# Optimization experiments

Measured on AMD Instinct MI355X. Metric: run time of the kernel, lower is better.

The kernel has to match this reference:

```python
import jax, jax.numpy as jnp
import numpy as np

D_MODEL = 1024
N_HEADS = 16
D_HEAD = D_MODEL // N_HEADS
HIDDEN = 4096
B, T = 2, 2048
EPS = 1e-5


def setup_inputs() -> dict:
    key = jax.random.key(0)
    ks = jax.random.split(key, 16)
    s = 0.02
    return {
        "x": jax.random.normal(ks[0], (B, T, D_MODEL), dtype=jnp.float32),
        # LayerNorm 1
        "gamma1": jnp.ones((D_MODEL,), jnp.float32),
        "beta1": jnp.zeros((D_MODEL,), jnp.float32),
        # attention projections, stored (in, out) so y = x @ W + b
        "Wq": jax.random.normal(ks[1], (D_MODEL, D_MODEL), jnp.float32) * s,
        "bq": jnp.zeros((D_MODEL,), jnp.float32),
        "Wk": jax.random.normal(ks[2], (D_MODEL, D_MODEL), jnp.float32) * s,
        "bk": jnp.zeros((D_MODEL,), jnp.float32),
        "Wv": jax.random.normal(ks[3], (D_MODEL, D_MODEL), jnp.float32) * s,
        "bv": jnp.zeros((D_MODEL,), jnp.float32),
        "Wo": jax.random.normal(ks[4], (D_MODEL, D_MODEL), jnp.float32) * s,
        "bo": jnp.zeros((D_MODEL,), jnp.float32),
        # LayerNorm 2
        "gamma2": jnp.ones((D_MODEL,), jnp.float32),
        "beta2": jnp.zeros((D_MODEL,), jnp.float32),
        # MLP
        "W1": jax.random.normal(ks[5], (D_MODEL, HIDDEN), jnp.float32) * s,
        "b1": jnp.zeros((HIDDEN,), jnp.float32),
        "W2": jax.random.normal(ks[6], (HIDDEN, D_MODEL), jnp.float32) * s,
        "b2": jnp.zeros((D_MODEL,), jnp.float32),
    }


def _layernorm(x, gamma, beta):
    mean = jnp.mean(x, axis=-1, keepdims=True)
    var = jnp.mean(jnp.square(x - mean), axis=-1, keepdims=True)  # unbiased=False
    return gamma * (x - mean) * jax.lax.rsqrt(var + EPS) + beta


def _attention(x, Wq, bq, Wk, bk, Wv, bv, Wo, bo):
    b, t, _ = x.shape
    q = (x @ Wq + bq).reshape(b, t, N_HEADS, D_HEAD)
    k = (x @ Wk + bk).reshape(b, t, N_HEADS, D_HEAD)
    v = (x @ Wv + bv).reshape(b, t, N_HEADS, D_HEAD)
    scores = jnp.einsum("bqhd,bkhd->bhqk", q, k) / np.sqrt(D_HEAD).astype(np.float32)
    causal = jnp.tril(jnp.ones((t, t), dtype=bool))  # keep j <= i
    scores = jnp.where(causal, scores, -jnp.inf)
    attn = jax.nn.softmax(scores, axis=-1)
    out = jnp.einsum("bhqk,bkhd->bqhd", attn, v).reshape(b, t, D_MODEL)
    return out @ Wo + bo


def reference(x, gamma1, beta1, Wq, bq, Wk, bk, Wv, bv, Wo, bo,
              gamma2, beta2, W1, b1, W2, b2):
    # x = x + Attn(LN1(x))
    x = x + _attention(_layernorm(x, gamma1, beta1), Wq, bq, Wk, bk, Wv, bv, Wo, bo)
    # x = x + MLP(LN2(x)); torch F.gelu default = exact erf gelu
    h = _layernorm(x, gamma2, beta2)
    h = jax.nn.gelu(h @ W1 + b1, approximate=False) @ W2 + b2
    return x + h
```

## Files before the change

kernel.cpp:

```cpp
#include <hip/hip_runtime.h>
#include <stdint.h>

typedef unsigned short u16;
typedef short bf16x8 __attribute__((ext_vector_type(8)));
typedef float f32x4 __attribute__((ext_vector_type(4)));
typedef float f32x16 __attribute__((ext_vector_type(16)));

#define MB (1024L*1024L)

__device__ inline u16 f2bf(float f) {
  union { float f; unsigned u; } v; v.f = f;
  unsigned r = (v.u + 0x7FFFu + ((v.u >> 16) & 1u)) >> 16;
  return (u16)r;
}

__device__ inline float bf2f(u16 u) {
  union { unsigned u; float f; } v; v.u = ((unsigned)u) << 16; return v.f;
}

__device__ inline unsigned cvtpk(float lo, float hi) {
  unsigned r;
  asm("v_cvt_pk_bf16_f32 %0, %1, %2" : "=v"(r) : "v"(lo), "v"(hi));
  return r;
}

#define GLOAD16(gptr, lptr) \
  __builtin_amdgcn_global_load_lds((__attribute__((address_space(1))) void*)(gptr), \
                                   (__attribute__((address_space(3))) void*)(lptr), 16, 0, 0)

__global__ __launch_bounds__(256) void twconv(const float* __restrict__ W,
                                              u16* __restrict__ WT, int K, int N) {
  __shared__ float tile[32][33];
  const int nbn = N >> 5;
  const int bk = blockIdx.x / nbn;
  const int bn = blockIdx.x % nbn;
  const int tid = threadIdx.x;
  const int r = tid >> 3;
  const int c4 = (tid & 7) << 2;
  const float4 v = *(const float4*)(W + (size_t)(bk * 32 + r) * N + bn * 32 + c4);
  tile[r][c4 + 0] = v.x; tile[r][c4 + 1] = v.y;
  tile[r][c4 + 2] = v.z; tile[r][c4 + 3] = v.w;
  __syncthreads();
  ushort4 o;
  o.x = f2bf(tile[c4 + 0][r]); o.y = f2bf(tile[c4 + 1][r]);
  o.z = f2bf(tile[c4 + 2][r]); o.w = f2bf(tile[c4 + 3][r]);
  *(ushort4*)(WT + (size_t)(bn * 32 + r) * K + bk * 32 + c4) = o;
}

__global__ __launch_bounds__(256) void concat3(const float* __restrict__ a,
                                               const float* __restrict__ b,
                                               const float* __restrict__ c,
                                               float* __restrict__ out, int n) {
  int i = blockIdx.x * 256 + threadIdx.x;
  if (i < n) { out[i] = a[i]; out[n + i] = b[i]; out[2 * n + i] = c[i]; }
}

__global__ __launch_bounds__(256) void ln_kernel(const float* __restrict__ x,
                                                 const float* __restrict__ gamma,
                                                 const float* __restrict__ beta,
                                                 u16* __restrict__ out) {
  const int row = blockIdx.x;
  const int tid = threadIdx.x;
  const float4 v = *(const float4*)(x + (size_t)row * 1024 + tid * 4);
  float s = v.x + v.y + v.z + v.w;
  float s2 = v.x * v.x + v.y * v.y + v.z * v.z + v.w * v.w;
#pragma unroll
  for (int m = 1; m < 64; m <<= 1) {
    s += __shfl_xor(s, m, 64);
    s2 += __shfl_xor(s2, m, 64);
  }
  __shared__ float red[8];
  const int w = tid >> 6;
  if ((tid & 63) == 0) { red[w] = s; red[4 + w] = s2; }
  __syncthreads();
  s = red[0] + red[1] + red[2] + red[3];
  s2 = red[4] + red[5] + red[6] + red[7];
  const float mean = s * (1.0f / 1024.0f);
  const float var = s2 * (1.0f / 1024.0f) - mean * mean;
  const float rstd = rsqrtf(var + 1e-5f);
  const float4 g = *(const float4*)(gamma + tid * 4);
  const float4 b = *(const float4*)(beta + tid * 4);
  ushort4 o;
  o.x = f2bf(g.x * (v.x - mean) * rstd + b.x);
  o.y = f2bf(g.y * (v.y - mean) * rstd + b.y);
  o.z = f2bf(g.z * (v.z - mean) * rstd + b.z);
  o.w = f2bf(g.w * (v.w - mean) * rstd + b.w);
  *(ushort4*)(out + (size_t)row * 1024 + tid * 4) = o;
}

template <int EPI, int BN>
__global__ __launch_bounds__(256, (BN == 64) ? 3 : 2)
void gemm_bt(const u16* __restrict__ A, const u16* __restrict__ BT,
             const float* __restrict__ bias, const float* __restrict__ res,
             void* __restrict__ outp, int M, int N, int K) {
  constexpr int MF = (BN == 128) ? 4 : 2;
  constexpr int ACH = 4;
  constexpr int BCH = BN / 32;
  constexpr int LOADS = ACH + BCH;
  __shared__ __align__(16) u16 As[2][128 * 64];
  __shared__ __align__(16) u16 Bs[2][BN * 64];
  const int nBN = N / BN;
  const int hw = blockIdx.x;
  const int xcd = hw & 7;
  const int rr = hw >> 3;
  const int bm = xcd * 4 + rr / nBN;
  const int bn = rr % nBN;
  const int tid = threadIdx.x;
  const int lane = tid & 63;
  const int wid = tid >> 6;
  const int wm = (BN == 128) ? (wid >> 1) : wid;
  const int wn = (BN == 128) ? (wid & 1) : 0;
  const int e4 = lane >> 4;

  int abase[MF], ax[MF];
#pragma unroll
  for (int m = 0; m < MF; ++m) {
    int rowa = wm * (MF * 16) + m * 16 + (lane & 15);
    abase[m] = rowa * 64; ax[m] = rowa & 7;
  }
  int bbase[4], bx[4];
#pragma unroll
  for (int n = 0; n < 4; ++n) {
    int rowb = wn * 64 + n * 16 + (lane & 15);
    bbase[n] = rowb * 64; bx[n] = rowb & 7;
  }

  size_t ga[ACH]; int loa[ACH];
#pragma unroll
  for (int c = 0; c < ACH; ++c) {
    int idx = tid + (c << 8);
    int row = idx >> 3;
    int ch = (idx & 7) ^ (row & 7);
    ga[c] = (size_t)(bm * 128 + row) * K + (ch << 3);
    loa[c] = idx << 4;
  }
  size_t gb[BCH]; int lob[BCH];
#pragma unroll
  for (int c = 0; c < BCH; ++c) {
    int idx = tid + (c << 8);
    int row = idx >> 3;
    int ch = (idx & 7) ^ (row & 7);
    gb[c] = (size_t)(bn * BN + row) * K + (ch << 3);
    lob[c] = idx << 4;
  }

#define STAGE_G(t, bb) do { \
  _Pragma("unroll") for (int c = 0; c < ACH; ++c) \
    GLOAD16(A + ga[c] + (size_t)(t) * 64, (char*)As[bb] + loa[c]); \
  _Pragma("unroll") for (int c = 0; c < BCH; ++c) \
    GLOAD16(BT + gb[c] + (size_t)(t) * 64, (char*)Bs[bb] + lob[c]); \
} while (0)

  f32x4 acc[MF][4] = {};
  const int nt = K >> 6;

  STAGE_G(0, 0);
  STAGE_G(1, 1);

  for (int t = 0; t < nt; ++t) {
    if (t + 1 < nt) {
      asm volatile("s_waitcnt vmcnt(%0)" :: "i"(LOADS) : "memory");
    } else {
      asm volatile("s_waitcnt vmcnt(0)" ::: "memory");
    }
    __builtin_amdgcn_s_barrier();
    const u16* Ap = As[t & 1];
    const u16* Bp = Bs[t & 1];
    bf16x8 af[2][MF], bfr[2][4];
#pragma unroll
    for (int kk = 0; kk < 2; ++kk) {
#pragma unroll
      for (int m = 0; m < MF; ++m)
        af[kk][m] = *(const bf16x8*)(Ap + abase[m] + (((((kk << 2) | e4)) ^ ax[m]) << 3));
#pragma unroll
      for (int n = 0; n < 4; ++n)
        bfr[kk][n] = *(const bf16x8*)(Bp + bbase[n] + (((((kk << 2) | e4)) ^ bx[n]) << 3));
    }
    asm volatile("s_waitcnt lgkmcnt(0)" ::: "memory");
    __builtin_amdgcn_s_barrier();
    if (t + 2 < nt) STAGE_G(t + 2, t & 1);
    __builtin_amdgcn_s_setprio(1);
#pragma unroll
    for (int kk = 0; kk < 2; ++kk)
#pragma unroll
      for (int m = 0; m < MF; ++m)
#pragma unroll
        for (int n = 0; n < 4; ++n)
          acc[m][n] = __builtin_amdgcn_mfma_f32_16x16x32_bf16(af[kk][m], bfr[kk][n], acc[m][n], 0, 0, 0);
    __builtin_amdgcn_s_setprio(0);
  }
#undef STAGE_G

  const int rbase = bm * 128 + wm * (MF * 16);
  const int cbase = bn * BN + wn * 64;
#pragma unroll
  for (int m = 0; m < MF; ++m) {
#pragma unroll
    for (int n = 0; n < 4; ++n) {
      const int col = cbase + n * 16 + (lane & 15);
      const int row0 = rbase + m * 16 + ((lane >> 4) << 2);
      const float bv = bias[col];
#pragma unroll
      for (int r = 0; r < 4; ++r) {
        const int row = row0 + r;
        float v = acc[m][n][r] + bv;
        if (EPI == 1) {
          ((float*)outp)[(size_t)row * N + col] = v + res[(size_t)row * N + col];
        } else if (EPI == 2) {
          float tt = v * (1.0f + 0.044715f * v * v);
          float sg = 1.0f / (1.0f + __expf(-1.5957691216057308f * tt));
          ((u16*)outp)[(size_t)row * N + col] = f2bf(v * sg);
        } else {
          ((u16*)outp)[(size_t)row * N + col] = f2bf(v);
        }
      }
    }
  }
}

__global__ __launch_bounds__(256, 3) void attn_kernel(const u16* __restrict__ QKV,
                                                      u16* __restrict__ O) {
  __shared__ __align__(16) u16 KV[4][4096];
  const int T = 2048, LD = 3072;
  const int hw = blockIdx.x;
  const int xcd = hw & 7;
  const int rr = hw >> 3;
  const int bh = xcd + 8 * (rr >> 4);
  const int p = rr & 15;
  const int b = bh >> 4, hd = bh & 15;
  const int tid = threadIdx.x;
  const int lane = tid & 63;
  const int w = tid >> 6;
  const int h = lane >> 5;
  const int cA = p, cB = 31 - p;
  const int myc = (w < 2) ? cA : cB;
  const int qwb = myc * 64 + (w & 1) * 32;
  const int qg = qwb + (lane & 31);
  const int myNt = myc + 1;
  const int nt = cB + 1;

  const u16* Qb = QKV + (size_t)b * T * LD + hd * 64;
  const u16* Kb = Qb + 1024;
  const u16* Vb = Qb + 2048;

  const float QSC = 0.18033688011112042f;
  bf16x8 qf[4];
#pragma unroll
  for (int s = 0; s < 4; ++s) {
    bf16x8 raw = *(const bf16x8*)(Qb + (size_t)qg * LD + s * 16 + h * 8);
    union { unsigned wd[4]; bf16x8 v; } u;
#pragma unroll
    for (int e = 0; e < 4; ++e)
      u.wd[e] = cvtpk(bf2f((u16)raw[2 * e]) * QSC, bf2f((u16)raw[2 * e + 1]) * QSC);
    qf[s] = u.v;
  }

  f32x16 oacc[2] = {};
  float m = -INFINITY, l = 0.0f;

  int krow[2], kgc[2], vrow[2], vcol[2];
#pragma unroll
  for (int c2 = 0; c2 < 2; ++c2) {
    int idx = tid + (c2 << 8);
    krow[c2] = idx >> 3;
    kgc[c2] = ((idx & 7) ^ (krow[c2] & 7)) << 3;
    vrow[c2] = idx >> 3;
    vcol[c2] = idx & 7;
  }

#pragma unroll
  for (int c2 = 0; c2 < 2; ++c2) {
    GLOAD16(Kb + (size_t)krow[c2] * LD + kgc[c2], (char*)KV[0] + (tid + (c2 << 8)) * 16);
    bf16x8 vv0 = *(const bf16x8*)(Vb + (size_t)vrow[c2] * LD + vcol[c2] * 8);
#pragma unroll
    for (int e = 0; e < 8; ++e) {
      int d = vcol[c2] * 8 + e;
      KV[2][(d << 6) | (vrow[c2] & 7) | ((((vrow[c2] >> 3) ^ e ^ vcol[c2]) & 7) << 3)] = (u16)vv0[e];
    }
  }
  __syncthreads();

  int cur = 0;
  for (int j = 0; j < nt; ++j) {
    const bool pre = (j + 1 < nt);
    bf16x8 vv[2];
    if (pre) {
#pragma unroll
      for (int c2 = 0; c2 < 2; ++c2) {
        GLOAD16(Kb + (size_t)((j + 1) * 64 + krow[c2]) * LD + kgc[c2],
                (char*)KV[cur ^ 1] + (tid + (c2 << 8)) * 16);
        vv[c2] = *(const bf16x8*)(Vb + (size_t)((j + 1) * 64 + vrow[c2]) * LD + vcol[c2] * 8);
      }
    }

    if (j < myNt) {
      f32x16 sacc[2] = {};
      const u16* Kp = KV[cur];
#pragma unroll
      for (int t = 0; t < 2; ++t) {
#pragma unroll
        for (int s = 0; s < 4; ++s) {
          int row = t * 32 + (lane & 31);
          bf16x8 kf = *(const bf16x8*)(Kp + (row << 6) + ((((2 * s + h) ^ (row & 7)) & 7) << 3));
          sacc[t] = __builtin_amdgcn_mfma_f32_32x32x16_bf16(kf, qf[s], sacc[t], 0, 0, 0);
        }
      }

      if (j == myc) {
#pragma unroll
        for (int t = 0; t < 2; ++t)
#pragma unroll
          for (int r = 0; r < 16; ++r) {
            int key = (j << 6) + 32 * t + (r & 3) + 8 * (r >> 2) + 4 * h;
            if (key > qg) sacc[t][r] = -INFINITY;
          }
      }

      float pmax = -INFINITY;
#pragma unroll
      for (int t = 0; t < 2; ++t)
#pragma unroll
        for (int r = 0; r < 16; ++r) pmax = fmaxf(pmax, sacc[t][r]);
      pmax = fmaxf(pmax, __shfl_xor(pmax, 32, 64));

      if (!__all(pmax - m <= 2.8853900817779268f)) {
        float mn = fmaxf(m, pmax);
        float alpha = exp2f(m - mn);
        m = mn;
        l *= alpha;
#pragma unroll
        for (int d2 = 0; d2 < 2; ++d2)
#pragma unroll
          for (int r = 0; r < 16; ++r) oacc[d2][r] *= alpha;
      }

      float lsum = 0.0f;
#pragma unroll
      for (int t = 0; t < 2; ++t)
#pragma unroll
        for (int r = 0; r < 16; ++r) {
          float pe = exp2f(sacc[t][r] - m);
          sacc[t][r] = pe;
          lsum += pe;
        }
      lsum += __shfl_xor(lsum, 32, 64);
      l += lsum;

      union PF { unsigned wd[4]; bf16x8 v; } pf[4];
#pragma unroll
      for (int t = 0; t < 2; ++t) {
#pragma unroll
        for (int kb = 0; kb < 2; ++kb) {
          int base = 8 * kb;
          unsigned A0 = cvtpk(sacc[t][base + 0], sacc[t][base + 1]);
          unsigned A2 = cvtpk(sacc[t][base + 2], sacc[t][base + 3]);
          unsigned A4 = cvtpk(sacc[t][base + 4], sacc[t][base + 5]);
          unsigned A6 = cvtpk(sacc[t][base + 6], sacc[t][base + 7]);
          unsigned S0 = (unsigned)__shfl_xor((int)(h ? A0 : A4), 32, 64);
          unsigned S2 = (unsigned)__shfl_xor((int)(h ? A2 : A6), 32, 64);
          PF& u = pf[2 * t + kb];
          u.wd[0] = h ? S0 : A0;
          u.wd[1] = h ? S2 : A2;
          u.wd[2] = h ? A4 : S0;
          u.wd[3] = h ? A6 : S2;
        }
      }

      const u16* Vp = KV[2 + cur];
#pragma unroll
      for (int d2 = 0; d2 < 2; ++d2) {
        int d = d2 * 32 + (lane & 31);
#pragma unroll
        for (int ks = 0; ks < 4; ++ks) {
          bf16x8 vf = *(const bf16x8*)(Vp + (d << 6) + ((((2 * ks + h) ^ (d & 7) ^ ((d >> 3) & 7)) & 7) << 3));
          oacc[d2] = __builtin_amdgcn_mfma_f32_32x32x16_bf16(vf, pf[ks].v, oacc[d2], 0, 0, 0);
        }
      }
    }

    if (pre) {
#pragma unroll
      for (int c2 = 0; c2 < 2; ++c2)
#pragma unroll
        for (int e = 0; e < 8; ++e) {
          int d = vcol[c2] * 8 + e;
          KV[2 + (cur ^ 1)][(d << 6) | (vrow[c2] & 7) | ((((vrow[c2] >> 3) ^ e ^ vcol[c2]) & 7) << 3)] = (u16)vv[c2][e];
        }
    }
    __syncthreads();
    cur ^= 1;
  }

  const float rinv = 1.0f / l;
  u16* Ob = (u16*)KV;
  const int qloc = w * 32 + (lane & 31);
#pragma unroll
  for (int d2 = 0; d2 < 2; ++d2)
#pragma unroll
    for (int r = 0; r < 16; ++r) {
      int d = d2 * 32 + (r & 3) + 8 * (r >> 2) + 4 * h;
      Ob[(qloc << 6) | (d ^ ((qloc & 7) << 3))] = f2bf(oacc[d2][r] * rinv);
    }
  __syncthreads();
#pragma unroll
  for (int it = 0; it < 4; ++it) {
    int r = (tid >> 3) + it * 32;
    int c = tid & 7;
    bf16x8 val = *(const bf16x8*)(Ob + (r << 6) + (((c ^ (r & 7)) & 7) << 3));
    int qg2 = (r < 64) ? (cA * 64 + r) : (cB * 64 + (r - 64));
    *(bf16x8*)(O + (size_t)(b * T + qg2) * 1024 + hd * 64 + c * 8) = val;
  }
}

extern "C" void kernel_launch(void* const* d_in, const int* in_sizes, int n_in,
                              void* d_out, int out_size, void* d_ws, size_t ws_size,
                              hipStream_t stream) {
  const float* x      = (const float*)d_in[0];
  const float* gamma1 = (const float*)d_in[1];
  const float* beta1  = (const float*)d_in[2];
  const float* Wq     = (const float*)d_in[3];
  const float* bq     = (const float*)d_in[4];
  const float* Wk     = (const float*)d_in[5];
  const float* bk     = (const float*)d_in[6];
  const float* Wv     = (const float*)d_in[7];
  const float* bv     = (const float*)d_in[8];
  const float* Wo     = (const float*)d_in[9];
  const float* bo     = (const float*)d_in[10];
  const float* gamma2 = (const float*)d_in[11];
  const float* beta2  = (const float*)d_in[12];
  const float* W1     = (const float*)d_in[13];
  const float* b1     = (const float*)d_in[14];
  const float* W2     = (const float*)d_in[15];
  const float* b2     = (const float*)d_in[16];

  char* ws = (char*)d_ws;
  u16* WqkvT = (u16*)(ws + 0 * MB);
  u16* WoT   = (u16*)(ws + 6 * MB);
  u16* W1T   = (u16*)(ws + 8 * MB);
  u16* W2T   = (u16*)(ws + 16 * MB);
  u16* qkv   = (u16*)(ws + 24 * MB);
  u16* hb    = (u16*)(ws + 24 * MB);
  u16* xn    = (u16*)(ws + 56 * MB);
  float* bqkv = (float*)d_out;
  float* x1 = (float*)d_out;

  const int M = 4096;

  twconv<<<dim3(1024), dim3(256), 0, stream>>>(Wq, WqkvT, 1024, 1024);
  twconv<<<dim3(1024), dim3(256), 0, stream>>>(Wk, WqkvT + 1024 * 1024, 1024, 1024);
  twconv<<<dim3(1024), dim3(256), 0, stream>>>(Wv, WqkvT + 2048 * 1024, 1024, 1024);
  twconv<<<dim3(1024), dim3(256), 0, stream>>>(Wo, WoT, 1024, 1024);
  twconv<<<dim3(4096), dim3(256), 0, stream>>>(W1, W1T, 1024, 4096);
  twconv<<<dim3(4096), dim3(256), 0, stream>>>(W2, W2T, 4096, 1024);
  concat3<<<dim3(4), dim3(256), 0, stream>>>(bq, bk, bv, bqkv, 1024);

  ln_kernel<<<dim3(M), dim3(256), 0, stream>>>(x, gamma1, beta1, xn);

  gemm_bt<0, 128><<<dim3(768), dim3(256), 0, stream>>>(xn, WqkvT, bqkv, nullptr, qkv, M, 3072, 1024);

  attn_kernel<<<dim3(512), dim3(256), 0, stream>>>(qkv, xn);

  gemm_bt<1, 64><<<dim3(512), dim3(256), 0, stream>>>(xn, WoT, bo, x, x1, M, 1024, 1024);

  ln_kernel<<<dim3(M), dim3(256), 0, stream>>>(x1, gamma2, beta2, xn);

  gemm_bt<2, 128><<<dim3(1024), dim3(256), 0, stream>>>(xn, W1T, b1, nullptr, hb, M, 4096, 1024);
  gemm_bt<1, 64><<<dim3(512), dim3(256), 0, stream>>>(hb, W2T, b2, x1, d_out, M, 1024, 4096);
}
```

Baseline: 254.3 us.

## Enlarge attention tiles to 128 queries/keys with 512-thread blocks

Restructures the causal flash-attention kernel so each block has 8 waves covering two 128-row query chunks, and processes 128-key K/V tiles per iteration instead of 64. The V transpose swizzle is widened to 16 groups for the new row stride, and the block-to-head mapping is changed so each XCD handles 4 heads. s_setprio is raised around the MFMA sections. The aim is more K/V reuse per shared-memory load and fewer barriers. The cost is a grid of only 256 blocks, which may leave CUs underused, plus more LDS and registers per block.

Result: no change. 252.3 us (-0.8%).

```diff
diff --git a/kernel.cpp b/kernel.cpp
--- a/kernel.cpp
+++ b/kernel.cpp
@@ -218,24 +218,24 @@
   }
 }
 
-__global__ __launch_bounds__(256, 3) void attn_kernel(const u16* __restrict__ QKV,
+__global__ __launch_bounds__(512, 2) void attn_kernel(const u16* __restrict__ QKV,
                                                       u16* __restrict__ O) {
-  __shared__ __align__(16) u16 KV[4][4096];
+  __shared__ __align__(16) u16 Ks[2][8192];
+  __shared__ __align__(16) u16 Vt[2][8192];
   const int T = 2048, LD = 3072;
-  const int hw = blockIdx.x;
-  const int xcd = hw & 7;
-  const int rr = hw >> 3;
-  const int bh = xcd + 8 * (rr >> 4);
-  const int p = rr & 15;
+  const int blk = blockIdx.x;
+  const int xcd = blk & 7;
+  const int idx = blk >> 3;
+  const int bh = xcd * 4 + (idx & 3);
+  const int p = idx >> 2;
   const int b = bh >> 4, hd = bh & 15;
   const int tid = threadIdx.x;
   const int lane = tid & 63;
   const int w = tid >> 6;
   const int h = lane >> 5;
-  const int cA = p, cB = 31 - p;
-  const int myc = (w < 2) ? cA : cB;
-  const int qwb = myc * 64 + (w & 1) * 32;
-  const int qg = qwb + (lane & 31);
+  const int cA = p, cB = 15 - p;
+  const int myc = (w < 4) ? cA : cB;
+  const int qg = myc * 128 + (w & 3) * 32 + (lane & 31);
   const int myNt = myc + 1;
   const int nt = cB + 1;
 
@@ -261,22 +261,25 @@
   int krow[2], kgc[2], vrow[2], vcol[2];
 #pragma unroll
   for (int c2 = 0; c2 < 2; ++c2) {
-    int idx = tid + (c2 << 8);
-    krow[c2] = idx >> 3;
-    kgc[c2] = ((idx & 7) ^ (krow[c2] & 7)) << 3;
-    vrow[c2] = idx >> 3;
-    vcol[c2] = idx & 7;
-  }
+    int i2 = tid + (c2 << 9);
+    krow[c2] = i2 >> 3;
+    kgc[c2] = ((i2 & 7) ^ (krow[c2] & 7)) << 3;
+    vrow[c2] = i2 >> 3;
+    vcol[c2] = i2 & 7;
+  }
+
+#define VWRITE(bb, c2, vvreg) do { \
+  _Pragma("unroll") for (int e = 0; e < 8; ++e) { \
+    int d = vcol[c2] * 8 + e; \
+    Vt[bb][(d << 7) | (vrow[c2] & 7) | ((((vrow[c2] >> 3) ^ (d & 15)) & 15) << 3)] = (u16)(vvreg)[e]; \
+  } \
+} while (0)
 
 #pragma unroll
   for (int c2 = 0; c2 < 2; ++c2) {
-    GLOAD16(Kb + (size_t)krow[c2] * LD + kgc[c2], (char*)KV[0] + (tid + (c2 << 8)) * 16);
+    GLOAD16(Kb + (size_t)krow[c2] * LD + kgc[c2], (char*)Ks[0] + (tid + (c2 << 9)) * 16);
     bf16x8 vv0 = *(const bf16x8*)(Vb + (size_t)vrow[c2] * LD + vcol[c2] * 8);
-#pragma unroll
-    for (int e = 0; e < 8; ++e) {
-      int d = vcol[c2] * 8 + e;
-      KV[2][(d << 6) | (vrow[c2] & 7) | ((((vrow[c2] >> 3) ^ e ^ vcol[c2]) & 7) << 3)] = (u16)vv0[e];
-    }
+    VWRITE(0, c2, vv0);
   }
   __syncthreads();
 
@@ -287,17 +290,18 @@
     if (pre) {
 #pragma unroll
       for (int c2 = 0; c2 < 2; ++c2) {
-        GLOAD16(Kb + (size_t)((j + 1) * 64 + krow[c2]) * LD + kgc[c2],
-                (char*)KV[cur ^ 1] + (tid + (c2 << 8)) * 16);
-        vv[c2] = *(const bf16x8*)(Vb + (size_t)((j + 1) * 64 + vrow[c2]) * LD + vcol[c2] * 8);
+        GLOAD16(Kb + (size_t)((j + 1) * 128 + krow[c2]) * LD + kgc[c2],
+                (char*)Ks[cur ^ 1] + (tid + (c2 << 9)) * 16);
+        vv[c2] = *(const bf16x8*)(Vb + (size_t)((j + 1) * 128 + vrow[c2]) * LD + vcol[c2] * 8);
       }
     }
 
     if (j < myNt) {
-      f32x16 sacc[2] = {};
-      const u16* Kp = KV[cur];
-#pragma unroll
-      for (int t = 0; t < 2; ++t) {
+      f32x16 sacc[4] = {};
+      const u16* Kp = Ks[cur];
+      __builtin_amdgcn_s_setprio(1);
+#pragma unroll
+      for (int t = 0; t < 4; ++t) {
 #pragma unroll
         for (int s = 0; s < 4; ++s) {
           int row = t * 32 + (lane & 31);
@@ -305,20 +309,21 @@
           sacc[t] = __builtin_amdgcn_mfma_f32_32x32x16_bf16(kf, qf[s], sacc[t], 0, 0, 0);
         }
       }
+      __builtin_amdgcn_s_setprio(0);
 
       if (j == myc) {
 #pragma unroll
-        for (int t = 0; t < 2; ++t)
+        for (int t = 0; t < 4; ++t)
 #pragma unroll
           for (int r = 0; r < 16; ++r) {
-            int key = (j << 6) + 32 * t + (r & 3) + 8 * (r >> 2) + 4 * h;
+            int key = (j << 7) + 32 * t + (r & 3) + 8 * (r >> 2) + 4 * h;
             if (key > qg) sacc[t][r] = -INFINITY;
           }
       }
 
       float pmax = -INFINITY;
 #pragma unroll
-      for (int t = 0; t < 2; ++t)
+      for (int t = 0; t < 4; ++t)
 #pragma unroll
         for (int r = 0; r < 16; ++r) pmax = fmaxf(pmax, sacc[t][r]);
       pmax = fmaxf(pmax, __shfl_xor(pmax, 32, 64));
@@ -336,7 +341,7 @@
 
       float lsum = 0.0f;
 #pragma unroll
-      for (int t = 0; t < 2; ++t)
+      for (int t = 0; t < 4; ++t)
 #pragma unroll
         for (int r = 0; r < 16; ++r) {
           float pe = exp2f(sacc[t][r] - m);
@@ -346,9 +351,9 @@
       lsum += __shfl_xor(lsum, 32, 64);
       l += lsum;
 
-      union PF { unsigned wd[4]; bf16x8 v; } pf[4];
-#pragma unroll
-      for (int t = 0; t < 2; ++t) {
+      union PF { unsigned wd[4]; bf16x8 v; } pf[8];
+#pragma unroll
+      for (int t = 0; t < 4; ++t) {
 #pragma unroll
         for (int kb = 0; kb < 2; ++kb) {
           int base = 8 * kb;
@@ -366,33 +371,31 @@
         }
       }
 
-      const u16* Vp = KV[2 + cur];
+      const u16* Vp = Vt[cur];
+      __builtin_amdgcn_s_setprio(1);
 #pragma unroll
       for (int d2 = 0; d2 < 2; ++d2) {
         int d = d2 * 32 + (lane & 31);
 #pragma unroll
-        for (int ks = 0; ks < 4; ++ks) {
-          bf16x8 vf = *(const bf16x8*)(Vp + (d << 6) + ((((2 * ks + h) ^ (d & 7) ^ ((d >> 3) & 7)) & 7) << 3));
+        for (int ks = 0; ks < 8; ++ks) {
+          bf16x8 vf = *(const bf16x8*)(Vp + (d << 7) + ((((2 * ks + h) ^ (d & 15)) & 15) << 3));
           oacc[d2] = __builtin_amdgcn_mfma_f32_32x32x16_bf16(vf, pf[ks].v, oacc[d2], 0, 0, 0);
         }
       }
+      __builtin_amdgcn_s_setprio(0);
     }
 
     if (pre) {
 #pragma unroll
-      for (int c2 = 0; c2 < 2; ++c2)
-#pragma unroll
-        for (int e = 0; e < 8; ++e) {
-          int d = vcol[c2] * 8 + e;
-          KV[2 + (cur ^ 1)][(d << 6) | (vrow[c2] & 7) | ((((vrow[c2] >> 3) ^ e ^ vcol[c2]) & 7) << 3)] = (u16)vv[c2][e];
-        }
+      for (int c2 = 0; c2 < 2; ++c2) VWRITE(cur ^ 1, c2, vv[c2]);
     }
     __syncthreads();
     cur ^= 1;
   }
+#undef VWRITE
 
   const float rinv = 1.0f / l;
-  u16* Ob = (u16*)KV;
+  u16* Ob = (u16*)Ks;
   const int qloc = w * 32 + (lane & 31);
 #pragma unroll
   for (int d2 = 0; d2 < 2; ++d2)
@@ -404,10 +407,10 @@
   __syncthreads();
 #pragma unroll
   for (int it = 0; it < 4; ++it) {
-    int r = (tid >> 3) + it * 32;
+    int r = (tid >> 3) + it * 64;
     int c = tid & 7;
     bf16x8 val = *(const bf16x8*)(Ob + (r << 6) + (((c ^ (r & 7)) & 7) << 3));
-    int qg2 = (r < 64) ? (cA * 64 + r) : (cB * 64 + (r - 64));
+    int qg2 = (r < 128) ? (cA * 128 + r) : (cB * 128 + (r - 128));
     *(bf16x8*)(O + (size_t)(b * T + qg2) * 1024 + hd * 64 + c * 8) = val;
   }
 }
@@ -458,7 +461,7 @@
 
   gemm_bt<0, 128><<<dim3(768), dim3(256), 0, stream>>>(xn, WqkvT, bqkv, nullptr, qkv, M, 3072, 1024);
 
-  attn_kernel<<<dim3(512), dim3(256), 0, stream>>>(qkv, xn);
+  attn_kernel<<<dim3(256), dim3(512), 0, stream>>>(qkv, xn);
 
   gemm_bt<1, 64><<<dim3(512), dim3(256), 0, stream>>>(xn, WoT, bo, x, x1, M, 1024, 1024);
 
```
